# Performance work log

Measured on AMD Instinct MI355X. Metric: run time of the kernel, lower is better.

## Reference

```python
import jax, jax.numpy as jnp
import numpy as np

K = 32  # sae_k

def setup_inputs() -> dict:
    key = jax.random.key(0)
    k1, k2, k3 = jax.random.split(key, 3)
    B, D, H = 8192, 256, 8192  # batch, d_in, hidden_dim = d_in * scale_size
    x = jax.random.normal(k1, (B, D), dtype=jnp.float32)
    W_enc = jax.random.normal(k2, (H, D), dtype=jnp.float32) * (1.0 / np.sqrt(D))
    b_enc = jnp.zeros((H,), dtype=jnp.float32)
    # W_dec initialized as clone of encoder weight then row-normalized to unit norm
    W_dec = jax.random.normal(k3, (H, D), dtype=jnp.float32)
    W_dec = W_dec / (jnp.linalg.norm(W_dec, axis=1, keepdims=True) + jnp.finfo(jnp.float32).eps)
    b_dec = jnp.zeros((D,), dtype=jnp.float32)
    return {"x": x, "W_enc": W_enc, "b_enc": b_enc, "W_dec": W_dec, "b_dec": b_dec}

def reference(x, W_enc, b_enc, W_dec, b_dec):
    # sae_in = x - b_dec; pre_acts = relu(encoder(sae_in))
    sae_in = x - b_dec
    pre_acts = jax.nn.relu(jnp.einsum('bd,hd->bh', sae_in, W_enc) + b_enc)  # [B, H]
    # top-k activation: keep k largest latents per row, zero the rest
    topk_vals, topk_idx = jax.lax.top_k(pre_acts, K)  # [B, K]
    B = pre_acts.shape[0]
    rows = jnp.arange(B)[:, None]
    z = jnp.zeros_like(pre_acts).at[rows, topk_idx].set(topk_vals)  # sparse activation [B, H]
    # decode
    x_reconstructed = jnp.einsum('bh,hd->bd', z, W_dec) + b_dec
    return x_reconstructed
```

## Files before the change

### kernel.cpp

```cpp
#include <hip/hip_runtime.h>

#define DIN   256
#define HID   8192
#define BATCH 8192
#define TOPK  32
#define BM    32
#define HHALF 4096
#define NCH   16
#define NS1   48
#define MRG   96
#define NS2   40
#define AS_LD 264
#define XF_LD 260
#define CAP   112
#define K2_LD 113
#define WCAP  352
#define THRM  0.1375f
#define DBM   4
#define DT    256
#define GK_OFF ((size_t)4 << 20)

typedef __bf16 bf16x8 __attribute__((ext_vector_type(8)));
typedef unsigned short u16x8 __attribute__((ext_vector_type(8)));
typedef float f32x4v __attribute__((ext_vector_type(4)));

__device__ __forceinline__ unsigned short f2bf(float f) {
  unsigned x = __builtin_bit_cast(unsigned, f);
  x = x + 0x7fffu + ((x >> 16) & 1u);
  return (unsigned short)(x >> 16);
}

__global__ __launch_bounds__(512) void wenc_cast(
    const float* __restrict__ Wenc, unsigned short* __restrict__ wsb)
{
  const int g = (int)blockIdx.x * 512 + (int)threadIdx.x;
  const int h = g >> 5, u = g & 31, kg = u >> 2, quad = u & 3;
  const float* src = Wenc + (size_t)h * DIN + kg * 32 + quad * 8;
  float4 a = *(const float4*)src;
  float4 b = *(const float4*)(src + 4);
  u16x8 o;
  o[0] = f2bf(a.x); o[1] = f2bf(a.y); o[2] = f2bf(a.z); o[3] = f2bf(a.w);
  o[4] = f2bf(b.x); o[5] = f2bf(b.y); o[6] = f2bf(b.z); o[7] = f2bf(b.w);
  *(u16x8*)(wsb + ((size_t)(((h >> 4) * 8 + kg) * 64 + quad * 16 + (h & 15))) * 8) = o;
}

__global__ __launch_bounds__(512) __attribute__((amdgpu_waves_per_eu(4)))
void sae_enc(
    const float* __restrict__ x,    const float* __restrict__ benc,
    const float* __restrict__ bdec, const unsigned short* __restrict__ wsb,
    unsigned* __restrict__ gkeys)
{
  __shared__ __align__(16) union UA {
    unsigned short As[BM][AS_LD];
    struct { unsigned wkey[8][WCAP]; unsigned char wrow[8][WCAP]; } w;
  } ua;
  __shared__ unsigned keys2[BM][K2_LD];
  __shared__ __align__(16) float benc_l[HHALF];
  __shared__ int   cnt[BM];
  __shared__ float rthr[BM];
  __shared__ int   wn[8];

  const int tid  = (int)threadIdx.x;
  const int wave = tid >> 6;
  const int lane = tid & 63;
  const int quad = lane >> 4;
  const int ln15 = lane & 15;
  const int rt   = (int)blockIdx.x >> 1;
  const int hs   = (int)blockIdx.x & 1;
  const int mb   = rt * BM;

  {
    const int r = tid >> 4, seg = tid & 15;
    const float* xs = x + (size_t)(mb + r) * DIN + seg * 16;
    const float* bs = bdec + seg * 16;
    float ss = 0.0f;
    #pragma unroll
    for (int j = 0; j < 4; ++j) {
      float4 xv = *(const float4*)(xs + 4 * j);
      float4 bv = *(const float4*)(bs + 4 * j);
      float dx = xv.x - bv.x, dy = xv.y - bv.y;
      float dz = xv.z - bv.z, dw = xv.w - bv.w;
      ss += dx * dx + dy * dy + dz * dz + dw * dw;
      unsigned short* dst = &ua.As[r][seg * 16 + 4 * j];
      dst[0] = f2bf(dx); dst[1] = f2bf(dy);
      dst[2] = f2bf(dz); dst[3] = f2bf(dw);
    }
    #pragma unroll
    for (int d = 1; d < 16; d <<= 1) ss += __shfl_xor(ss, d, 16);
    if (seg == 0) { rthr[r] = THRM * sqrtf(ss); cnt[r] = 0; }
  }
  {
    const float* bsrc = benc + hs * HHALF + tid * 8;
    float4 b0 = *(const float4*)bsrc;
    float4 b1 = *(const float4*)(bsrc + 4);
    *(float4*)&benc_l[tid * 8]     = b0;
    *(float4*)&benc_l[tid * 8 + 4] = b1;
  }
  __syncthreads();

  bf16x8 afrag[2][8];
  #pragma unroll
  for (int mt = 0; mt < 2; ++mt)
    #pragma unroll
    for (int gk = 0; gk < 8; ++gk)
      afrag[mt][gk] = *(const bf16x8*)&ua.As[mt * 16 + ln15][gk * 32 + quad * 8];

  float thr[8];
  #pragma unroll
  for (int s = 0; s < 8; ++s) thr[s] = rthr[(s >> 2) * 16 + quad * 4 + (s & 3)];
  __syncthreads();

  unsigned wbase = 0;

  for (int c = 0; c < NCH; ++c) {
    const unsigned short* bp =
        wsb + (((size_t)(hs * 256 + c * 16 + wave * 2) * 512) + lane) * 8;
    #pragma unroll
    for (int nt = 0; nt < 2; ++nt) {
      bf16x8 bfrag[8];
      #pragma unroll
      for (int kg = 0; kg < 8; ++kg)
        bfrag[kg] = *(const bf16x8*)(bp + (size_t)nt * 4096 + (size_t)kg * 512);

      const int hwl = c * 256 + (wave * 2 + nt) * 16 + ln15;
      const float be = benc_l[hwl];
      f32x4v acc[2];
      #pragma unroll
      for (int mt = 0; mt < 2; ++mt)
        #pragma unroll
        for (int i = 0; i < 4; ++i) acc[mt][i] = be;

      __builtin_amdgcn_s_setprio(1);
      #pragma unroll
      for (int kg = 0; kg < 8; ++kg) {
        acc[0] = __builtin_amdgcn_mfma_f32_16x16x32_bf16(afrag[0][kg], bfrag[kg], acc[0], 0, 0, 0);
        acc[1] = __builtin_amdgcn_mfma_f32_16x16x32_bf16(afrag[1][kg], bfrag[kg], acc[1], 0, 0, 0);
      }
      __builtin_amdgcn_s_setprio(0);

      const unsigned idxpart = (unsigned)(8191 - (hs * HHALF + hwl));
      #pragma unroll
      for (int s = 0; s < 8; ++s) {
        const int mt = s >> 2, i = s & 3;
        const bool take = acc[mt][i] > thr[s];
        const unsigned long long bm = __ballot(take);
        if (take) {
          const int pos = (int)wbase + __popcll(bm & ((1ull << lane) - 1ull));
          if (pos < WCAP) {
            ua.w.wkey[wave][pos] = ((unsigned)f2bf(acc[mt][i]) << 16) | idxpart;
            ua.w.wrow[wave][pos] = (unsigned char)(mt * 16 + quad * 4 + i);
          }
        }
        wbase += (unsigned)__popcll(bm);
      }
    }
  }
  if (lane == 0) wn[wave] = (int)(wbase < WCAP ? wbase : WCAP);
  __syncthreads();

  for (int w = 0; w < 8; ++w) {
    const int n = wn[w];
    for (int e = tid; e < n; e += 512) {
      const unsigned k = ua.w.wkey[w][e];
      const int row = (int)ua.w.wrow[w][e];
      const int sl = atomicAdd(&cnt[row], 1);
      if (sl < CAP) keys2[row][sl] = k;
    }
  }
  __syncthreads();

  {
    const int row = tid >> 4, l16 = tid & 15;
    const int n = min(cnt[row], CAP);
    unsigned myk[CAP / 16];
    int rk[CAP / 16];
    #pragma unroll
    for (int j = 0; j < CAP / 16; ++j) {
      const int idx = l16 + 16 * j;
      myk[j] = (idx < n) ? keys2[row][idx] : 0u;
      rk[j] = 0;
    }
    for (int e = 0; e < n; ++e) {
      const unsigned k2 = keys2[row][e];
      #pragma unroll
      for (int j = 0; j < CAP / 16; ++j) rk[j] += (k2 > myk[j]) ? 1 : 0;
    }
    unsigned* gout = gkeys + (size_t)(mb + row) * MRG + hs * NS1;
    #pragma unroll
    for (int j = 0; j < CAP / 16; ++j) {
      const int idx = l16 + 16 * j;
      if (idx < n && rk[j] < NS1) gout[rk[j]] = myk[j];
    }
    if (l16 == 0)
      for (int p = n; p < NS1; ++p) gout[p] = (unsigned)(0x4000 + hs * 64 + p);
  }
}

__global__ __launch_bounds__(DT) void sae_dec(
    const float* __restrict__ x,    const float* __restrict__ Wenc,
    const float* __restrict__ benc, const float* __restrict__ Wdec,
    const float* __restrict__ bdec, const unsigned* __restrict__ gkeys,
    float* __restrict__ out)
{
  __shared__ unsigned mk[DBM][MRG];
  __shared__ __align__(16) float xf[DBM][XF_LD];
  __shared__ float tv[DBM][NS2];
  __shared__ int   ti[DBM][NS2];
  __shared__ float sv[DBM][TOPK];
  __shared__ int   si[DBM][TOPK];

  const int tid = (int)threadIdx.x;
  const int mb  = (int)blockIdx.x * DBM;

  #pragma unroll
  for (int i = tid; i < DBM * MRG; i += DT)
    mk[i / MRG][i % MRG] = gkeys[(size_t)mb * MRG + i];

  {
    const int r = tid >> 6, seg = tid & 63;
    float4 xv = *(const float4*)(x + (size_t)(mb + r) * DIN + seg * 4);
    float4 bv = *(const float4*)(bdec + seg * 4);
    float4 d;
    d.x = xv.x - bv.x; d.y = xv.y - bv.y; d.z = xv.z - bv.z; d.w = xv.w - bv.w;
    *(float4*)&xf[r][seg * 4] = d;
  }
  __syncthreads();

  if (tid < DBM * 32) {
    const int row = tid >> 5, l32 = tid & 31;
    unsigned myk[3];
    int rk[3];
    #pragma unroll
    for (int j = 0; j < 3; ++j) { myk[j] = mk[row][l32 + 32 * j]; rk[j] = 0; }
    for (int e = 0; e < MRG; ++e) {
      const unsigned k2 = mk[row][e];
      #pragma unroll
      for (int j = 0; j < 3; ++j) rk[j] += (k2 > myk[j]) ? 1 : 0;
    }
    #pragma unroll
    for (int j = 0; j < 3; ++j)
      if (rk[j] < NS2) ti[row][rk[j]] = 8191 - (int)(myk[j] & 0xFFFFu);
  }
  __syncthreads();

  {
    const int sub = tid & 15, task = tid >> 4;
    for (int p = 0; p < (DBM * NS2) / 16; ++p) {
      const int pp = p * 16 + task;
      const int row = pp / NS2, cand = pp - row * NS2;
      const int h = ti[row][cand];
      double a0 = 0.0, a1 = 0.0;
      if (h >= 0) {
        const float* wp = Wenc + (size_t)h * DIN + sub * 16;
        const float* xp = &xf[row][sub * 16];
        float4 w0 = *(const float4*)(wp);
        float4 w1 = *(const float4*)(wp + 4);
        float4 w2 = *(const float4*)(wp + 8);
        float4 w3 = *(const float4*)(wp + 12);
        float4 x0 = *(const float4*)(xp);
        float4 x1 = *(const float4*)(xp + 4);
        float4 x2 = *(const float4*)(xp + 8);
        float4 x3 = *(const float4*)(xp + 12);
        a0 += (double)x0.x * (double)w0.x + (double)x0.y * (double)w0.y;
        a1 += (double)x0.z * (double)w0.z + (double)x0.w * (double)w0.w;
        a0 += (double)x1.x * (double)w1.x + (double)x1.y * (double)w1.y;
        a1 += (double)x1.z * (double)w1.z + (double)x1.w * (double)w1.w;
        a0 += (double)x2.x * (double)w2.x + (double)x2.y * (double)w2.y;
        a1 += (double)x2.z * (double)w2.z + (double)x2.w * (double)w2.w;
        a0 += (double)x3.x * (double)w3.x + (double)x3.y * (double)w3.y;
        a1 += (double)x3.z * (double)w3.z + (double)x3.w * (double)w3.w;
      }
      double accd = a0 + a1;
      accd += __shfl_xor(accd, 8, 16);
      accd += __shfl_xor(accd, 4, 16);
      accd += __shfl_xor(accd, 2, 16);
      accd += __shfl_xor(accd, 1, 16);
      if (sub == 0) {
        float ev = (h >= 0) ? ((float)accd + benc[h]) : 0.0f;
        ev = ev > 0.0f ? ev : 0.0f;
        tv[row][cand] = ev;
      }
    }
  }
  __syncthreads();

  if (tid < DBM * NS2) {
    const int row = tid / NS2, cand = tid - row * NS2;
    const float v = tv[row][cand];
    const int   h = ti[row][cand];
    int rk = 0;
    for (int e = 0; e < NS2; ++e) {
      const float v2 = tv[row][e];
      const int   h2 = ti[row][e];
      rk += (v2 > v || (v2 == v && (unsigned)h2 < (unsigned)h)) ? 1 : 0;
    }
    if (rk < TOPK) { sv[row][rk] = v; si[row][rk] = h; }
  }
  __syncthreads();

  {
    const int r = tid >> 6, d0 = (tid & 63) * 4;
    float4 bb = *(const float4*)(bdec + d0);
    float o0 = bb.x, o1 = bb.y, o2 = bb.z, o3 = bb.w;
    #pragma unroll
    for (int s = 0; s < TOPK; ++s) {
      const float v = sv[r][s];
      const int   h = si[r][s];
      const float* wp = Wdec + (size_t)((v > 0.0f) ? h : 0) * DIN + d0;
      float4 w = *(const float4*)wp;
      o0 += v * w.x; o1 += v * w.y; o2 += v * w.z; o3 += v * w.w;
    }
    float4 o;
    o.x = o0; o.y = o1; o.z = o2; o.w = o3;
    *(float4*)(out + (size_t)(mb + r) * DIN + d0) = o;
  }
}

extern "C" void kernel_launch(void* const* d_in, const int* in_sizes, int n_in,
                              void* d_out, int out_size, void* d_ws, size_t ws_size,
                              hipStream_t stream) {
  const float* x    = (const float*)d_in[0];
  const float* Wenc = (const float*)d_in[1];
  const float* benc = (const float*)d_in[2];
  const float* Wdec = (const float*)d_in[3];
  const float* bdec = (const float*)d_in[4];
  float* out = (float*)d_out;
  unsigned short* wsb = (unsigned short*)d_ws;
  unsigned* gkeys = (unsigned*)((char*)d_ws + GK_OFF);

  wenc_cast<<<dim3((HID * DIN / 8) / 512), dim3(512), 0, stream>>>(Wenc, wsb);
  sae_enc<<<dim3(2 * BATCH / BM), dim3(512), 0, stream>>>(x, benc, bdec, wsb, gkeys);
  sae_dec<<<dim3(BATCH / DBM), dim3(DT), 0, stream>>>(x, Wenc, benc, Wdec, bdec, gkeys, out);
}
```

Measured before the change: 196.5 us.

## Fuse decode stage into encoder kernel via last-block-arrives atomic flag

Removes the separate decode kernel. Each pair of encoder blocks covering the same 32-row tile increments a per-tile flag, and the second block to finish runs the merge, the fp64 rescoring, the top-k and the decode for that tile, using a shared-memory union. This saves one kernel launch and lets decode work overlap with encoder blocks still running. In exchange, the tail runs in only half the blocks with 512 threads over 32 rows, and the flags must be reset by the cast kernel.

```diff
diff --git a/kernel.cpp b/kernel.cpp
--- a/kernel.cpp
+++ b/kernel.cpp
@@ -16,9 +16,8 @@
 #define K2_LD 113
 #define WCAP  352
 #define THRM  0.1375f
-#define DBM   4
-#define DT    256
 #define GK_OFF ((size_t)4 << 20)
+#define FL_OFF (GK_OFF + ((size_t)3 << 20))
 
 typedef __bf16 bf16x8 __attribute__((ext_vector_type(8)));
 typedef unsigned short u16x8 __attribute__((ext_vector_type(8)));
@@ -31,8 +30,10 @@
 }
 
 __global__ __launch_bounds__(512) void wenc_cast(
-    const float* __restrict__ Wenc, unsigned short* __restrict__ wsb)
+    const float* __restrict__ Wenc, unsigned short* __restrict__ wsb,
+    unsigned* __restrict__ flags)
 {
+  if (blockIdx.x == 0 && threadIdx.x < 256) flags[threadIdx.x] = 0u;
   const int g = (int)blockIdx.x * 512 + (int)threadIdx.x;
   const int h = g >> 5, u = g & 31, kg = u >> 2, quad = u & 3;
   const float* src = Wenc + (size_t)h * DIN + kg * 32 + quad * 8;
@@ -44,21 +45,39 @@
   *(u16x8*)(wsb + ((size_t)(((h >> 4) * 8 + kg) * 64 + quad * 16 + (h & 15))) * 8) = o;
 }
 
+struct AsW {
+  union {
+    unsigned short As[BM][AS_LD];
+    struct { unsigned wkey[8][WCAP]; unsigned char wrow[8][WCAP]; } w;
+  } ua;
+};
+struct GemmSh {
+  AsW a;
+  unsigned keys2[BM][K2_LD];
+  float benc_l[HHALF];
+};
+struct TailSh {
+  float xf[BM][XF_LD];
+  unsigned mk[BM][MRG];
+  float tv[BM][NS2];
+  int   ti[BM][NS2];
+  float sv[BM][TOPK];
+  int   si[BM][TOPK];
+};
+
 __global__ __launch_bounds__(512) __attribute__((amdgpu_waves_per_eu(4)))
 void sae_enc(
     const float* __restrict__ x,    const float* __restrict__ benc,
     const float* __restrict__ bdec, const unsigned short* __restrict__ wsb,
-    unsigned* __restrict__ gkeys)
+    unsigned* __restrict__ gkeys,   const float* __restrict__ Wenc,
+    const float* __restrict__ Wdec, float* __restrict__ out,
+    unsigned* __restrict__ flags)
 {
-  __shared__ __align__(16) union UA {
-    unsigned short As[BM][AS_LD];
-    struct { unsigned wkey[8][WCAP]; unsigned char wrow[8][WCAP]; } w;
-  } ua;
-  __shared__ unsigned keys2[BM][K2_LD];
-  __shared__ __align__(16) float benc_l[HHALF];
+  __shared__ __align__(16) union { GemmSh g; TailSh t; } u;
   __shared__ int   cnt[BM];
   __shared__ float rthr[BM];
   __shared__ int   wn[8];
+  __shared__ unsigned oldv_sh;
 
   const int tid  = (int)threadIdx.x;
   const int wave = tid >> 6;
@@ -81,7 +100,7 @@
       float dx = xv.x - bv.x, dy = xv.y - bv.y;
       float dz = xv.z - bv.z, dw = xv.w - bv.w;
       ss += dx * dx + dy * dy + dz * dz + dw * dw;
-      unsigned short* dst = &ua.As[r][seg * 16 + 4 * j];
+      unsigned short* dst = &u.g.a.ua.As[r][seg * 16 + 4 * j];
       dst[0] = f2bf(dx); dst[1] = f2bf(dy);
       dst[2] = f2bf(dz); dst[3] = f2bf(dw);
     }
@@ -93,8 +112,8 @@
     const float* bsrc = benc + hs * HHALF + tid * 8;
     float4 b0 = *(const float4*)bsrc;
     float4 b1 = *(const float4*)(bsrc + 4);
-    *(float4*)&benc_l[tid * 8]     = b0;
-    *(float4*)&benc_l[tid * 8 + 4] = b1;
+    *(float4*)&u.g.benc_l[tid * 8]     = b0;
+    *(float4*)&u.g.benc_l[tid * 8 + 4] = b1;
   }
   __syncthreads();
 
@@ -103,7 +122,7 @@
   for (int mt = 0; mt < 2; ++mt)
     #pragma unroll
     for (int gk = 0; gk < 8; ++gk)
-      afrag[mt][gk] = *(const bf16x8*)&ua.As[mt * 16 + ln15][gk * 32 + quad * 8];
+      afrag[mt][gk] = *(const bf16x8*)&u.g.a.ua.As[mt * 16 + ln15][gk * 32 + quad * 8];
 
   float thr[8];
   #pragma unroll
@@ -123,7 +142,7 @@
         bfrag[kg] = *(const bf16x8*)(bp + (size_t)nt * 4096 + (size_t)kg * 512);
 
       const int hwl = c * 256 + (wave * 2 + nt) * 16 + ln15;
-      const float be = benc_l[hwl];
+      const float be = u.g.benc_l[hwl];
       f32x4v acc[2];
       #pragma unroll
       for (int mt = 0; mt < 2; ++mt)
@@ -147,8 +166,8 @@
         if (take) {
           const int pos = (int)wbase + __popcll(bm & ((1ull << lane) - 1ull));
           if (pos < WCAP) {
-            ua.w.wkey[wave][pos] = ((unsigned)f2bf(acc[mt][i]) << 16) | idxpart;
-            ua.w.wrow[wave][pos] = (unsigned char)(mt * 16 + quad * 4 + i);
+            u.g.a.ua.w.wkey[wave][pos] = ((unsigned)f2bf(acc[mt][i]) << 16) | idxpart;
+            u.g.a.ua.w.wrow[wave][pos] = (unsigned char)(mt * 16 + quad * 4 + i);
           }
         }
         wbase += (unsigned)__popcll(bm);
@@ -161,10 +180,10 @@
   for (int w = 0; w < 8; ++w) {
     const int n = wn[w];
     for (int e = tid; e < n; e += 512) {
-      const unsigned k = ua.w.wkey[w][e];
-      const int row = (int)ua.w.wrow[w][e];
+      const unsigned k = u.g.a.ua.w.wkey[w][e];
+      const int row = (int)u.g.a.ua.w.wrow[w][e];
       const int sl = atomicAdd(&cnt[row], 1);
-      if (sl < CAP) keys2[row][sl] = k;
+      if (sl < CAP) u.g.keys2[row][sl] = k;
     }
   }
   __syncthreads();
@@ -177,11 +196,11 @@
     #pragma unroll
     for (int j = 0; j < CAP / 16; ++j) {
       const int idx = l16 + 16 * j;
-      myk[j] = (idx < n) ? keys2[row][idx] : 0u;
+      myk[j] = (idx < n) ? u.g.keys2[row][idx] : 0u;
       rk[j] = 0;
     }
     for (int e = 0; e < n; ++e) {
-      const unsigned k2 = keys2[row][e];
+      const unsigned k2 = u.g.keys2[row][e];
       #pragma unroll
       for (int j = 0; j < CAP / 16; ++j) rk[j] += (k2 > myk[j]) ? 1 : 0;
     }
@@ -194,65 +213,56 @@
     if (l16 == 0)
       for (int p = n; p < NS1; ++p) gout[p] = (unsigned)(0x4000 + hs * 64 + p);
   }
-}
-
-__global__ __launch_bounds__(DT) void sae_dec(
-    const float* __restrict__ x,    const float* __restrict__ Wenc,
-    const float* __restrict__ benc, const float* __restrict__ Wdec,
-    const float* __restrict__ bdec, const unsigned* __restrict__ gkeys,
-    float* __restrict__ out)
-{
-  __shared__ unsigned mk[DBM][MRG];
-  __shared__ __align__(16) float xf[DBM][XF_LD];
-  __shared__ float tv[DBM][NS2];
-  __shared__ int   ti[DBM][NS2];
-  __shared__ float sv[DBM][TOPK];
-  __shared__ int   si[DBM][TOPK];
-
-  const int tid = (int)threadIdx.x;
-  const int mb  = (int)blockIdx.x * DBM;
-
-  #pragma unroll
-  for (int i = tid; i < DBM * MRG; i += DT)
-    mk[i / MRG][i % MRG] = gkeys[(size_t)mb * MRG + i];
-
-  {
-    const int r = tid >> 6, seg = tid & 63;
+
+  __syncthreads();
+  if (tid == 0) {
+    __threadfence();
+    oldv_sh = atomicAdd(&flags[rt], 1u);
+  }
+  __syncthreads();
+  if (oldv_sh != 1u) return;
+  if (tid == 0) __threadfence();
+  __syncthreads();
+
+  for (int i = tid; i < BM * MRG; i += 512)
+    u.t.mk[i / MRG][i % MRG] = gkeys[(size_t)mb * MRG + i];
+  for (int i = tid; i < BM * 64; i += 512) {
+    const int r = i >> 6, seg = i & 63;
     float4 xv = *(const float4*)(x + (size_t)(mb + r) * DIN + seg * 4);
     float4 bv = *(const float4*)(bdec + seg * 4);
     float4 d;
     d.x = xv.x - bv.x; d.y = xv.y - bv.y; d.z = xv.z - bv.z; d.w = xv.w - bv.w;
-    *(float4*)&xf[r][seg * 4] = d;
-  }
-  __syncthreads();
-
-  if (tid < DBM * 32) {
-    const int row = tid >> 5, l32 = tid & 31;
-    unsigned myk[3];
-    int rk[3];
-    #pragma unroll
-    for (int j = 0; j < 3; ++j) { myk[j] = mk[row][l32 + 32 * j]; rk[j] = 0; }
+    *(float4*)&u.t.xf[r][seg * 4] = d;
+  }
+  __syncthreads();
+
+  {
+    const int row = tid >> 4, l16 = tid & 15;
+    unsigned myk[6];
+    int rk[6];
+    #pragma unroll
+    for (int j = 0; j < 6; ++j) { myk[j] = u.t.mk[row][l16 + 16 * j]; rk[j] = 0; }
     for (int e = 0; e < MRG; ++e) {
-      const unsigned k2 = mk[row][e];
-      #pragma unroll
-      for (int j = 0; j < 3; ++j) rk[j] += (k2 > myk[j]) ? 1 : 0;
-    }
-    #pragma unroll
-    for (int j = 0; j < 3; ++j)
-      if (rk[j] < NS2) ti[row][rk[j]] = 8191 - (int)(myk[j] & 0xFFFFu);
+      const unsigned k2 = u.t.mk[row][e];
+      #pragma unroll
+      for (int j = 0; j < 6; ++j) rk[j] += (k2 > myk[j]) ? 1 : 0;
+    }
+    #pragma unroll
+    for (int j = 0; j < 6; ++j)
+      if (rk[j] < NS2) u.t.ti[row][rk[j]] = 8191 - (int)(myk[j] & 0xFFFFu);
   }
   __syncthreads();
 
   {
     const int sub = tid & 15, task = tid >> 4;
-    for (int p = 0; p < (DBM * NS2) / 16; ++p) {
-      const int pp = p * 16 + task;
+    for (int p = 0; p < (BM * NS2) / 32; ++p) {
+      const int pp = p * 32 + task;
       const int row = pp / NS2, cand = pp - row * NS2;
-      const int h = ti[row][cand];
+      const int h = u.t.ti[row][cand];
       double a0 = 0.0, a1 = 0.0;
       if (h >= 0) {
         const float* wp = Wenc + (size_t)h * DIN + sub * 16;
-        const float* xp = &xf[row][sub * 16];
+        const float* xp = &u.t.xf[row][sub * 16];
         float4 w0 = *(const float4*)(wp);
         float4 w1 = *(const float4*)(wp + 4);
         float4 w2 = *(const float4*)(wp + 8);
@@ -278,34 +288,34 @@
       if (sub == 0) {
         float ev = (h >= 0) ? ((float)accd + benc[h]) : 0.0f;
         ev = ev > 0.0f ? ev : 0.0f;
-        tv[row][cand] = ev;
+        u.t.tv[row][cand] = ev;
       }
     }
   }
   __syncthreads();
 
-  if (tid < DBM * NS2) {
-    const int row = tid / NS2, cand = tid - row * NS2;
-    const float v = tv[row][cand];
-    const int   h = ti[row][cand];
+  for (int i = tid; i < BM * NS2; i += 512) {
+    const int row = i / NS2, cand = i - row * NS2;
+    const float v = u.t.tv[row][cand];
+    const int   h = u.t.ti[row][cand];
     int rk = 0;
     for (int e = 0; e < NS2; ++e) {
-      const float v2 = tv[row][e];
-      const int   h2 = ti[row][e];
+      const float v2 = u.t.tv[row][e];
+      const int   h2 = u.t.ti[row][e];
       rk += (v2 > v || (v2 == v && (unsigned)h2 < (unsigned)h)) ? 1 : 0;
     }
-    if (rk < TOPK) { sv[row][rk] = v; si[row][rk] = h; }
-  }
-  __syncthreads();
-
-  {
-    const int r = tid >> 6, d0 = (tid & 63) * 4;
+    if (rk < TOPK) { u.t.sv[row][rk] = v; u.t.si[row][rk] = h; }
+  }
+  __syncthreads();
+
+  for (int i = tid; i < BM * 64; i += 512) {
+    const int r = i >> 6, d0 = (i & 63) * 4;
     float4 bb = *(const float4*)(bdec + d0);
     float o0 = bb.x, o1 = bb.y, o2 = bb.z, o3 = bb.w;
     #pragma unroll
     for (int s = 0; s < TOPK; ++s) {
-      const float v = sv[r][s];
-      const int   h = si[r][s];
+      const float v = u.t.sv[r][s];
+      const int   h = u.t.si[r][s];
       const float* wp = Wdec + (size_t)((v > 0.0f) ? h : 0) * DIN + d0;
       float4 w = *(const float4*)wp;
       o0 += v * w.x; o1 += v * w.y; o2 += v * w.z; o3 += v * w.w;
@@ -327,8 +337,9 @@
   float* out = (float*)d_out;
   unsigned short* wsb = (unsigned short*)d_ws;
   unsigned* gkeys = (unsigned*)((char*)d_ws + GK_OFF);
-
-  wenc_cast<<<dim3((HID * DIN / 8) / 512), dim3(512), 0, stream>>>(Wenc, wsb);
-  sae_enc<<<dim3(2 * BATCH / BM), dim3(512), 0, stream>>>(x, benc, bdec, wsb, gkeys);
-  sae_dec<<<dim3(BATCH / DBM), dim3(DT), 0, stream>>>(x, Wenc, benc, Wdec, bdec, gkeys, out);
+  unsigned* flags = (unsigned*)((char*)d_ws + FL_OFF);
+
+  wenc_cast<<<dim3((HID * DIN / 8) / 512), dim3(512), 0, stream>>>(Wenc, wsb, flags);
+  sae_enc<<<dim3(2 * BATCH / BM), dim3(512), 0, stream>>>(
+      x, benc, bdec, wsb, gkeys, Wenc, Wdec, out, flags);
 }
```

Measured after the change: 287.4 us. 1.46x slower.
